# Kernel tuning notes

Measured on AMD Instinct MI355X. Metric: run time of the kernel, lower is better.

The kernel has to match this reference:

```python
import jax, jax.numpy as jnp
import numpy as np

WD, WH, WW = 6, 6, 6
NUM_HEADS = 8
EPS = 1e-5


def setup_inputs() -> dict:
    key = jax.random.key(0)
    ks = jax.random.split(key, 4)
    B, C, D, H, W = 1, 128, 48, 48, 48
    return {
        "q_map": jax.random.normal(ks[0], (B, C, D, H, W), dtype=jnp.float32),
        "k_map": jax.random.normal(ks[1], (B, C, D, H, W), dtype=jnp.float32),
        "v_map": jax.random.normal(ks[2], (B, C, D, H, W), dtype=jnp.float32),
        "gamma_q": jnp.ones((C,), jnp.float32),
        "beta_q": jnp.zeros((C,), jnp.float32),
        "gamma_kv": jnp.ones((C,), jnp.float32),
        "beta_kv": jnp.zeros((C,), jnp.float32),
        "proj_w": jax.random.normal(ks[3], (C, C), dtype=jnp.float32) * (1.0 / np.sqrt(C)),
        "proj_b": jnp.zeros((C,), jnp.float32),
    }


def _layernorm(x, g, b):
    m = jnp.mean(x, axis=-1, keepdims=True)
    v = jnp.mean(jnp.square(x - m), axis=-1, keepdims=True)
    return (x - m) * jax.lax.rsqrt(v + EPS) * g + b


def _window_partition(x):
    # x: (B, D, H, W, C) -> windows: (B*nD*nH*nW, wd*wh*ww, C)
    B, D, H, W, C = x.shape
    pd, ph, pw = (WD - D % WD) % WD, (WH - H % WH) % WH, (WW - W % WW) % WW
    if pd or ph or pw:
        x = jnp.pad(x, ((0, 0), (0, pd), (0, ph), (0, pw), (0, 0)))
    Dp, Hp, Wp = D + pd, H + ph, W + pw
    x = x.reshape(B, Dp // WD, WD, Hp // WH, WH, Wp // WW, WW, C)
    x = jnp.transpose(x, (0, 1, 3, 5, 2, 4, 6, 7))
    return x.reshape(-1, WD * WH * WW, C), (D, H, W, Dp, Hp, Wp)


def _window_reverse(windows, meta):
    D, H, W, Dp, Hp, Wp = meta
    C = windows.shape[-1]
    nD, nH, nW = Dp // WD, Hp // WH, Wp // WW
    B = windows.shape[0] // (nD * nH * nW)
    x = windows.reshape(B, nD, nH, nW, WD, WH, WW, C)
    x = jnp.transpose(x, (0, 1, 4, 2, 5, 3, 6, 7)).reshape(B, Dp, Hp, Wp, C)
    return x[:, :D, :H, :W, :]


def reference(q_map, k_map, v_map, gamma_q, beta_q, gamma_kv, beta_kv, proj_w, proj_b):
    # (B, C, D, H, W) -> (B, D, H, W, C)
    q_map = jnp.transpose(q_map, (0, 2, 3, 4, 1))
    k_map = jnp.transpose(k_map, (0, 2, 3, 4, 1))
    v_map = jnp.transpose(v_map, (0, 2, 3, 4, 1))

    q, meta = _window_partition(q_map)
    k, _ = _window_partition(k_map)
    v, _ = _window_partition(v_map)

    q = _layernorm(q, gamma_q, beta_q)
    k = _layernorm(k, gamma_kv, beta_kv)
    v = _layernorm(v, gamma_kv, beta_kv)

    Bw, Nq, C = q.shape
    dh = C // NUM_HEADS
    q = q.reshape(Bw, Nq, NUM_HEADS, dh)
    k = k.reshape(Bw, -1, NUM_HEADS, dh)
    v = v.reshape(Bw, -1, NUM_HEADS, dh)

    scale = 1.0 / np.sqrt(dh).astype(np.float32)
    scores = jnp.einsum("bqhd,bkhd->bhqk", q, k) * scale  # (Bw, h, Nq, Nk)
    attn = jax.nn.softmax(scores, axis=-1)
    out = jnp.einsum("bhqk,bkhd->bqhd", attn, v).reshape(Bw, Nq, C)

    out = out @ proj_w.T + proj_b
    out = _window_reverse(out, meta)
    return jnp.transpose(out, (0, 4, 1, 2, 3))  # (B, C, D, H, W)
```

## Files before the change

### kernel.cpp

```cpp
#include <hip/hip_runtime.h>
#include <hip/hip_bf16.h>

typedef short s16x8 __attribute__((ext_vector_type(8)));
typedef float f32x2 __attribute__((ext_vector_type(2)));
typedef float f32x4 __attribute__((ext_vector_type(4)));
typedef float f32x16 __attribute__((ext_vector_type(16)));
typedef unsigned int u32;
typedef unsigned short u16;
typedef u32 u32x4v __attribute__((ext_vector_type(4)));

#define TOK 216
#define THREADS 448
#define SP 110592
#define BUF0 0
#define VOFF 57344
#define WOFF 122880
#define GBOFF 155648
#define LDS_BYTES 157696

__device__ __forceinline__ u32 pack2(float a, float b) {
  u16 lo = __builtin_bit_cast(u16, __float2bfloat16(a));
  u16 hi = __builtin_bit_cast(u16, __float2bfloat16(b));
  return (u32)lo | ((u32)hi << 16);
}
__device__ __forceinline__ int swz(int row, int inner) {
  return inner ^ ((row & 7) << 4);
}

__device__ __forceinline__ void ln_stats(const f32x2* xv, float& mA, float& rA,
                                         float& mB, float& rB) {
  float sA = 0.f, s2A = 0.f, sB = 0.f, s2B = 0.f;
#pragma unroll
  for (int c = 0; c < 32; ++c) {
    sA += xv[c].x; s2A += xv[c].x * xv[c].x;
    sB += xv[c].y; s2B += xv[c].y * xv[c].y;
  }
  sA += __shfl_xor(sA, 1); s2A += __shfl_xor(s2A, 1);
  sB += __shfl_xor(sB, 1); s2B += __shfl_xor(s2B, 1);
  sA += __shfl_xor(sA, 2); s2A += __shfl_xor(s2A, 2);
  sB += __shfl_xor(sB, 2); s2B += __shfl_xor(s2B, 2);
  mA = sA * (1.0f / 128.0f);
  rA = rsqrtf(s2A * (1.0f / 128.0f) - mA * mA + 1e-5f);
  mB = sB * (1.0f / 128.0f);
  rB = rsqrtf(s2B * (1.0f / 128.0f) - mB * mB + 1e-5f);
}

template<bool MASK>
__device__ __forceinline__ void attn_step(const char* smem, int h, int kt,
                                          s16x8 qfh, int lane,
                                          f32x16& acc, float& lsum) {
  const int half = lane >> 5;
  const int krow = kt * 32 + (lane & 31);
  s16x8 kf = *(const s16x8*)(smem + BUF0 + krow * 256 +
                             swz(krow, h * 32 + half * 16));
  __builtin_amdgcn_s_setprio(1);
  f32x16 st = __builtin_amdgcn_mfma_f32_32x32x16_bf16(kf, qfh, (f32x16){}, 0, 0, 0);
  __builtin_amdgcn_s_setprio(0);
  const int vrow = h * 16 + (lane & 15);
  s16x8 vf0 = *(const s16x8*)(smem + VOFF + vrow * 512 +
                              swz(vrow, kt * 64 + half * 16));
  s16x8 vf1 = *(const s16x8*)(smem + VOFF + vrow * 512 +
                              swz(vrow, kt * 64 + 32 + half * 16));
  const int NR = MASK ? 12 : 16;
  u32 A[8];
  float ts = 0.f;
#pragma unroll
  for (int i = 0; i < 8; ++i) {
    float p0 = (2 * i < NR) ? __expf(st[2 * i]) : 0.f;
    float p1 = (2 * i + 1 < NR) ? __expf(st[2 * i + 1]) : 0.f;
    ts += p0 + p1;
    A[i] = pack2(p0, p1);
  }
  lsum += ts;
  s16x8 pf0 = __builtin_bit_cast(s16x8, (u32x4v){A[0], A[1], A[2], A[3]});
  s16x8 pf1 = __builtin_bit_cast(s16x8, (u32x4v){A[4], A[5], A[6], A[7]});
  __builtin_amdgcn_s_setprio(1);
  acc = __builtin_amdgcn_mfma_f32_32x32x16_bf16(vf0, pf0, acc, 0, 0, 0);
  acc = __builtin_amdgcn_mfma_f32_32x32x16_bf16(vf1, pf1, acc, 0, 0, 0);
  __builtin_amdgcn_s_setprio(0);
}

extern "C" __global__ __launch_bounds__(THREADS, 2)
void ca3d_kernel(const float* __restrict__ qm, const float* __restrict__ km,
                 const float* __restrict__ vm,
                 const float* __restrict__ gq, const float* __restrict__ bq,
                 const float* __restrict__ gkv, const float* __restrict__ bkv,
                 const float* __restrict__ pw, const float* __restrict__ pb,
                 float* __restrict__ out) {
  extern __shared__ __align__(16) char smem[];
  const int tid = threadIdx.x;
  const int lane = tid & 63;
  const int wv = tid >> 6;
  const int bid = blockIdx.x;
  const int wid = ((bid & 7) << 6) | (bid >> 3);
  const int wd = wid >> 6, wh = (wid >> 3) & 7, ww = wid & 7;
  const int boff = wd * 6 * 2304 + wh * 6 * 48 + ww * 6;

  for (int i = tid * 16; i < VOFF + 65536; i += THREADS * 16)
    *(f32x4*)(smem + i) = (f32x4){};
  if (tid < 128) {
    ((float*)(smem + GBOFF))[tid] = gq[tid];
    ((float*)(smem + GBOFF + 512))[tid] = bq[tid];
    ((float*)(smem + GBOFF + 1024))[tid] = gkv[tid];
    ((float*)(smem + GBOFF + 1536))[tid] = bkv[tid];
  }

  const bool lnAct = tid < 432;
  const int tp = tid >> 2;
  const int cbase = (tid & 3) * 32;
  const int tA = tp * 2, tB = tA + 1;
  int td = tA / 36, tr_ = tA - td * 36;
  int th_ = tr_ / 6, tw_ = tr_ - th_ * 6;
  const int gpos = boff + td * 2304 + th_ * 48 + tw_;
  const int vposA = (tA & ~0xC) | ((tA & 4) << 1) | ((tA & 8) >> 1);

  f32x2 qv[32], kv[32], vv[32];
  if (lnAct) {
#pragma unroll
    for (int c = 0; c < 32; ++c)
      qv[c] = *(const f32x2*)(qm + gpos + (cbase + c) * SP);
#pragma unroll
    for (int c = 0; c < 32; ++c)
      kv[c] = *(const f32x2*)(km + gpos + (cbase + c) * SP);
  }
  __syncthreads();

  const float* gql = (const float*)(smem + GBOFF);
  const float* bql = (const float*)(smem + GBOFF + 512);
  const float* gkl = (const float*)(smem + GBOFF + 1024);
  const float* bkl = (const float*)(smem + GBOFF + 1536);

  if (lnAct) {
    float mA, rA, mB, rB;
    ln_stats(qv, mA, rA, mB, rB);
#pragma unroll
    for (int c = 0; c < 32; c += 2) {
      int cc = cbase + c;
      float g0 = gql[cc], g1 = gql[cc + 1], b0 = bql[cc], b1 = bql[cc + 1];
      *(u32*)(smem + BUF0 + tA * 256 + swz(tA, cc * 2)) =
          pack2(((qv[c].x - mA) * rA * g0 + b0) * 0.25f,
                ((qv[c + 1].x - mA) * rA * g1 + b1) * 0.25f);
      *(u32*)(smem + BUF0 + tB * 256 + swz(tB, cc * 2)) =
          pack2(((qv[c].y - mB) * rB * g0 + b0) * 0.25f,
                ((qv[c + 1].y - mB) * rB * g1 + b1) * 0.25f);
    }
#pragma unroll
    for (int c = 0; c < 32; ++c)
      vv[c] = *(const f32x2*)(vm + gpos + (cbase + c) * SP);
  }
  __syncthreads();

  s16x8 qf[8];
  {
    int row = wv * 32 + (lane & 31);
    int ib = (lane >> 5) * 16;
#pragma unroll
    for (int h = 0; h < 8; ++h)
      qf[h] = *(const s16x8*)(smem + BUF0 + row * 256 + swz(row, h * 32 + ib));
  }
  __syncthreads();

  if (lnAct) {
    {
      float mA, rA, mB, rB;
      ln_stats(kv, mA, rA, mB, rB);
#pragma unroll
      for (int c = 0; c < 32; c += 2) {
        int cc = cbase + c;
        float g0 = gkl[cc], g1 = gkl[cc + 1], b0 = bkl[cc], b1 = bkl[cc + 1];
        *(u32*)(smem + BUF0 + tA * 256 + swz(tA, cc * 2)) =
            pack2((kv[c].x - mA) * rA * g0 + b0,
                  (kv[c + 1].x - mA) * rA * g1 + b1);
        *(u32*)(smem + BUF0 + tB * 256 + swz(tB, cc * 2)) =
            pack2((kv[c].y - mB) * rB * g0 + b0,
                  (kv[c + 1].y - mB) * rB * g1 + b1);
      }
    }
    {
      float mA, rA, mB, rB;
      ln_stats(vv, mA, rA, mB, rB);
#pragma unroll
      for (int c = 0; c < 32; ++c) {
        int cc = cbase + c;
        float g0 = gkl[cc], b0 = bkl[cc];
        *(u32*)(smem + VOFF + cc * 512 + swz(cc, vposA * 2)) =
            pack2((vv[c].x - mA) * rA * g0 + b0,
                  (vv[c].y - mB) * rB * g0 + b0);
      }
    }
  }
  for (int i = tid; i < 8192; i += THREADS) {
    int j = i >> 6, c2 = i & 63;
    f32x2 w2 = *(const f32x2*)(pw + j * 128 + c2 * 2);
    *(u32*)(smem + WOFF + j * 256 + swz(j, c2 * 4)) = pack2(w2.x, w2.y);
  }
  __syncthreads();

  u32 oPk[8][4];
#pragma unroll
  for (int hp = 0; hp < 4; ++hp) {
    const int h0 = hp * 2, h1 = h0 + 1;
    f32x16 a0 = {}, a1 = {};
    float l0 = 0.f, l1 = 0.f;
#pragma unroll 1
    for (int kt = 0; kt < 6; ++kt) {
      attn_step<false>(smem, h0, kt, qf[h0], lane, a0, l0);
      attn_step<false>(smem, h1, kt, qf[h1], lane, a1, l1);
    }
    attn_step<true>(smem, h0, 6, qf[h0], lane, a0, l0);
    attn_step<true>(smem, h1, 6, qf[h1], lane, a1, l1);
    l0 += __shfl_xor(l0, 32);
    l1 += __shfl_xor(l1, 32);
    float i0 = 1.0f / l0, i1 = 1.0f / l1;
#pragma unroll
    for (int r = 0; r < 4; ++r) {
      oPk[h0][r] = pack2(a0[2 * r] * i0, a0[2 * r + 1] * i0);
      oPk[h1][r] = pack2(a1[2 * r] * i1, a1[2 * r + 1] * i1);
    }
  }
  __syncthreads();

  {
    const int tok = wv * 32 + (lane & 31);
    const int half = lane >> 5;
#pragma unroll
    for (int h = 0; h < 8; ++h) {
      int chb = h * 32 + half * 8;
      *(u32*)(smem + BUF0 + tok * 256 + swz(tok, chb))      = oPk[h][0];
      *(u32*)(smem + BUF0 + tok * 256 + swz(tok, chb + 4))  = oPk[h][1];
      *(u32*)(smem + BUF0 + tok * 256 + swz(tok, chb + 16)) = oPk[h][2];
      *(u32*)(smem + BUF0 + tok * 256 + swz(tok, chb + 20)) = oPk[h][3];
    }
  }
  __syncthreads();

#pragma unroll 1
  for (int ti = 0; ti < 2; ++ti) {
    int tt = wv * 2 + ti;
    int tok = tt * 16 + (lane & 15);
    s16x8 bfr[4];
#pragma unroll
    for (int kk = 0; kk < 4; ++kk)
      bfr[kk] = *(const s16x8*)(smem + BUF0 + tok * 256 +
                                swz(tok, kk * 64 + (lane >> 4) * 16));
    bool tokValid = tok < TOK;
    int tdd = tok / 36, trr = tok - tdd * 36;
    int thh = trr / 6, tww = trr - thh * 6;
    int pos = boff + tdd * 2304 + thh * 48 + tww;
#pragma unroll 1
    for (int jt = 0; jt < 8; ++jt) {
      f32x4 acc = {};
#pragma unroll
      for (int kk = 0; kk < 4; ++kk) {
        int rw = jt * 16 + (lane & 15);
        s16x8 af = *(const s16x8*)(smem + WOFF + rw * 256 +
                                   swz(rw, kk * 64 + (lane >> 4) * 16));
        acc = __builtin_amdgcn_mfma_f32_16x16x32_bf16(af, bfr[kk], acc, 0, 0, 0);
      }
      f32x4 pbv = *(const f32x4*)(pb + jt * 16 + (lane >> 4) * 4);
      if (tokValid) {
#pragma unroll
        for (int r = 0; r < 4; ++r) {
          int j = jt * 16 + (lane >> 4) * 4 + r;
          out[j * SP + pos] = acc[r] + pbv[r];
        }
      }
    }
  }
}

extern "C" void kernel_launch(void* const* d_in, const int* in_sizes, int n_in,
                              void* d_out, int out_size, void* d_ws, size_t ws_size,
                              hipStream_t stream) {
  const float* qm  = (const float*)d_in[0];
  const float* km  = (const float*)d_in[1];
  const float* vm  = (const float*)d_in[2];
  const float* gq  = (const float*)d_in[3];
  const float* bq  = (const float*)d_in[4];
  const float* gkv = (const float*)d_in[5];
  const float* bkv = (const float*)d_in[6];
  const float* pw  = (const float*)d_in[7];
  const float* pb  = (const float*)d_in[8];
  hipLaunchKernelGGL(ca3d_kernel, dim3(512), dim3(THREADS), LDS_BYTES, stream,
                     qm, km, vm, gq, bq, gkv, bkv, pw, pb, (float*)d_out);
}
```

Measured before the change: 142.3 us.

## Split LayerNorm into bf16 pre-pass kernel and attention kernel with direct-to-LDS loads

Adds a pre-pass kernel that reads the fp32 channel-major q/k/v maps coalesced through shared memory, applies LayerNorm, and writes token-major bf16 tensors plus a bf16 projection weight into the workspace. The attention kernel then fills LDS with 16-byte global_load_lds copies, transposing V in LDS and zeroing its padding, instead of doing strided fp32 loads and LayerNorm in registers. The goal is better coalescing and fewer registers in the attention kernel. In exchange, roughly 85 MB of bf16 intermediates are written and read back, and a second kernel launch is added. The original fused kernel is kept as a fallback when the workspace is too small.

```diff
diff --git a/kernel.cpp b/kernel.cpp
--- a/kernel.cpp
+++ b/kernel.cpp
@@ -16,7 +16,10 @@
 #define VOFF 57344
 #define WOFF 122880
 #define GBOFF 155648
-#define LDS_BYTES 157696
+#define LDS_OLD 157696
+#define LDS_NEW 155648
+#define TENB 28311552ull
+#define WSNEED (3ull*TENB + 32768ull)
 
 __device__ __forceinline__ u32 pack2(float a, float b) {
   u16 lo = __builtin_bit_cast(u16, __float2bfloat16(a));
@@ -25,6 +28,11 @@
 }
 __device__ __forceinline__ int swz(int row, int inner) {
   return inner ^ ((row & 7) << 4);
+}
+__device__ __forceinline__ void gload16(const void* g, void* l) {
+  __builtin_amdgcn_global_load_lds(
+      (const __attribute__((address_space(1))) void*)g,
+      (__attribute__((address_space(3))) void*)l, 16, 0, 0);
 }
 
 __device__ __forceinline__ void ln_stats(const f32x2* xv, float& mA, float& rA,
@@ -80,6 +88,234 @@
   __builtin_amdgcn_s_setprio(0);
 }
 
+extern "C" __global__ __launch_bounds__(256)
+void lnpre_kernel(const float* __restrict__ qm, const float* __restrict__ km,
+                  const float* __restrict__ vm,
+                  const float* __restrict__ gq, const float* __restrict__ bq,
+                  const float* __restrict__ gkv, const float* __restrict__ bkv,
+                  const float* __restrict__ pw,
+                  u16* __restrict__ qn, u16* __restrict__ kn,
+                  u16* __restrict__ vn, u16* __restrict__ wbf) {
+  const int tid = threadIdx.x;
+  const int bid = blockIdx.x;
+  if (bid >= 2304) {
+#pragma unroll
+    for (int k = 0; k < 32; ++k) {
+      int idx = tid + 256 * k;
+      f32x2 w2 = *(const f32x2*)(pw + idx * 2);
+      ((u32*)wbf)[idx] = pack2(w2.x, w2.y);
+    }
+    return;
+  }
+  __shared__ float lf[6144];
+  __shared__ float gb[512];
+  const int d = bid / 48, h = bid - d * 48;
+  const int dh = d * 2304 + h * 48;
+  if (tid < 128) {
+    gb[tid] = gq[tid]; gb[128 + tid] = bq[tid];
+    gb[256 + tid] = gkv[tid]; gb[384 + tid] = bkv[tid];
+  }
+  const int w = tid >> 2, q = tid & 3;
+#pragma unroll 1
+  for (int t = 0; t < 3; ++t) {
+    const float* src = t == 0 ? qm : (t == 1 ? km : vm);
+    u16* dst = t == 0 ? qn : (t == 1 ? kn : vn);
+    const float* g = (t == 0) ? gb : gb + 256;
+    const float* b = (t == 0) ? gb + 128 : gb + 384;
+    const float scale = (t == 0) ? 0.25f : 1.0f;
+#pragma unroll
+    for (int k = 0; k < 6; ++k) {
+      int j = tid + 256 * k;
+      int ch = j / 12, wq = j - ch * 12;
+      *(f32x4*)(lf + ch * 48 + wq * 4) =
+          *(const f32x4*)(src + (long)ch * SP + dh + wq * 4);
+    }
+    __syncthreads();
+    if (tid < 192) {
+      float s = 0.f, s2 = 0.f;
+#pragma unroll
+      for (int c = 0; c < 32; ++c) {
+        float x = lf[(q + 4 * c) * 48 + w];
+        s += x; s2 += x * x;
+      }
+      s += __shfl_xor(s, 1); s2 += __shfl_xor(s2, 1);
+      s += __shfl_xor(s, 2); s2 += __shfl_xor(s2, 2);
+      float m = s * (1.f / 128.f);
+      float r = rsqrtf(s2 * (1.f / 128.f) - m * m + 1e-5f);
+      u32* op = (u32*)(dst + (long)(dh + w) * 128 + 32 * q);
+#pragma unroll
+      for (int cc = 0; cc < 32; cc += 2) {
+        int ch = 32 * q + cc;
+        float y0 = ((lf[ch * 48 + w] - m) * r * g[ch] + b[ch]) * scale;
+        float y1 = ((lf[(ch + 1) * 48 + w] - m) * r * g[ch + 1] + b[ch + 1]) * scale;
+        op[cc >> 1] = pack2(y0, y1);
+      }
+    }
+    __syncthreads();
+  }
+}
+
+extern "C" __global__ __launch_bounds__(THREADS, 2)
+void attn2_kernel(const u16* __restrict__ qn, const u16* __restrict__ kn,
+                  const u16* __restrict__ vn, const u16* __restrict__ wbf,
+                  const float* __restrict__ pb, float* __restrict__ out) {
+  extern __shared__ __align__(16) char smem[];
+  const int tid = threadIdx.x;
+  const int lane = tid & 63;
+  const int wv = tid >> 6;
+  const int bid = blockIdx.x;
+  const int wid = ((bid & 7) << 6) | (bid >> 3);
+  const int wd = wid >> 6, wh = (wid >> 3) & 7, ww = wid & 7;
+  const int wd6 = wd * 6, wh6 = wh * 6, ww6 = ww * 6;
+  const int boff = wd6 * 2304 + wh6 * 48 + ww6;
+
+  for (int uu = wv; uu < 140; uu += 7) {
+    const u16* s; char* d;
+    if (uu < 54) {
+      int u = uu, row = 4 * u + (lane >> 4);
+      int tq = row / 6;
+      int g = (wd6 + tq / 6) * 2304 + (wh6 + tq % 6) * 48 + ww6 + row % 6;
+      s = qn + g * 128 + (((lane & 15) ^ (row & 7)) << 3);
+      d = smem + BUF0 + u * 1024;
+    } else if (uu < 108) {
+      int u = uu - 54, row = 4 * u + (lane >> 4);
+      int tq = row / 6;
+      int g = (wd6 + tq / 6) * 2304 + (wh6 + tq % 6) * 48 + ww6 + row % 6;
+      s = vn + g * 128 + ((lane & 15) << 3);
+      d = smem + VOFF + u * 1024;
+    } else {
+      int u = uu - 108, row = 4 * u + (lane >> 4);
+      s = wbf + row * 128 + (((lane & 15) ^ (row & 7)) << 3);
+      d = smem + WOFF + u * 1024;
+    }
+    gload16(s, d);
+  }
+  __syncthreads();
+
+  s16x8 qf[8];
+  {
+    int row = wv * 32 + (lane & 31);
+    int ib = (lane >> 5) * 16;
+#pragma unroll
+    for (int h = 0; h < 8; ++h)
+      qf[h] = *(const s16x8*)(smem + BUF0 + row * 256 + swz(row, h * 32 + ib));
+  }
+  __syncthreads();
+
+  for (int uu = wv; uu < 54; uu += 7) {
+    int row = 4 * uu + (lane >> 4);
+    int tq = row / 6;
+    int g = (wd6 + tq / 6) * 2304 + (wh6 + tq % 6) * 48 + ww6 + row % 6;
+    gload16(kn + g * 128 + (((lane & 15) ^ (row & 7)) << 3),
+            smem + BUF0 + uu * 1024);
+  }
+  u32 tr[32];
+#pragma unroll
+  for (int k = 0; k < 16; ++k) {
+    int u = tid + 448 * k;
+    if (u < 6912) {
+      int t = (u >> 6) * 2, c2 = u & 63;
+      tr[2 * k]     = *(const u32*)(smem + VOFF + t * 256 + c2 * 4);
+      tr[2 * k + 1] = *(const u32*)(smem + VOFF + t * 256 + 256 + c2 * 4);
+    }
+  }
+  __syncthreads();
+
+#pragma unroll
+  for (int k = 0; k < 16; ++k) {
+    int u = tid + 448 * k;
+    if (u < 6912) {
+      int t = (u >> 6) * 2, c2 = u & 63;
+      int st = (t & ~12) | ((t & 4) << 1) | ((t & 8) >> 1);
+      int c = 2 * c2;
+      u32 w0 = (tr[2 * k] & 0xFFFFu) | (tr[2 * k + 1] << 16);
+      u32 w1 = (tr[2 * k] >> 16) | (tr[2 * k + 1] & 0xFFFF0000u);
+      *(u32*)(smem + VOFF + c * 512 + ((st * 2) ^ ((c & 7) << 4))) = w0;
+      *(u32*)(smem + VOFF + (c + 1) * 512 + ((st * 2) ^ (((c + 1) & 7) << 4))) = w1;
+    }
+  }
+  if (tid < 128) {
+    int x = (tid & 7) << 4;
+    *(u32*)(smem + VOFF + tid * 512 + (424 ^ x)) = 0;
+    *(u32*)(smem + VOFF + tid * 512 + (428 ^ x)) = 0;
+    *(u32*)(smem + VOFF + tid * 512 + (440 ^ x)) = 0;
+    *(u32*)(smem + VOFF + tid * 512 + (444 ^ x)) = 0;
+  }
+  __syncthreads();
+
+  u32 oPk[8][4];
+#pragma unroll
+  for (int hp = 0; hp < 4; ++hp) {
+    const int h0 = hp * 2, h1 = h0 + 1;
+    f32x16 a0 = {}, a1 = {};
+    float l0 = 0.f, l1 = 0.f;
+#pragma unroll 1
+    for (int kt = 0; kt < 6; ++kt) {
+      attn_step<false>(smem, h0, kt, qf[h0], lane, a0, l0);
+      attn_step<false>(smem, h1, kt, qf[h1], lane, a1, l1);
+    }
+    attn_step<true>(smem, h0, 6, qf[h0], lane, a0, l0);
+    attn_step<true>(smem, h1, 6, qf[h1], lane, a1, l1);
+    l0 += __shfl_xor(l0, 32);
+    l1 += __shfl_xor(l1, 32);
+    float i0 = 1.0f / l0, i1 = 1.0f / l1;
+#pragma unroll
+    for (int r = 0; r < 4; ++r) {
+      oPk[h0][r] = pack2(a0[2 * r] * i0, a0[2 * r + 1] * i0);
+      oPk[h1][r] = pack2(a1[2 * r] * i1, a1[2 * r + 1] * i1);
+    }
+  }
+  __syncthreads();
+
+  {
+    const int tok = wv * 32 + (lane & 31);
+    const int half = lane >> 5;
+#pragma unroll
+    for (int h = 0; h < 8; ++h) {
+      int chb = h * 32 + half * 8;
+      *(u32*)(smem + BUF0 + tok * 256 + swz(tok, chb))      = oPk[h][0];
+      *(u32*)(smem + BUF0 + tok * 256 + swz(tok, chb + 4))  = oPk[h][1];
+      *(u32*)(smem + BUF0 + tok * 256 + swz(tok, chb + 16)) = oPk[h][2];
+      *(u32*)(smem + BUF0 + tok * 256 + swz(tok, chb + 20)) = oPk[h][3];
+    }
+  }
+  __syncthreads();
+
+#pragma unroll 1
+  for (int ti = 0; ti < 2; ++ti) {
+    int tt = wv * 2 + ti;
+    int tok = tt * 16 + (lane & 15);
+    s16x8 bfr[4];
+#pragma unroll
+    for (int kk = 0; kk < 4; ++kk)
+      bfr[kk] = *(const s16x8*)(smem + BUF0 + tok * 256 +
+                                swz(tok, kk * 64 + (lane >> 4) * 16));
+    bool tokValid = tok < TOK;
+    int tdd = tok / 36, trr = tok - tdd * 36;
+    int thh = trr / 6, tww = trr - thh * 6;
+    int pos = boff + tdd * 2304 + thh * 48 + tww;
+#pragma unroll 1
+    for (int jt = 0; jt < 8; ++jt) {
+      f32x4 acc = {};
+#pragma unroll
+      for (int kk = 0; kk < 4; ++kk) {
+        int rw = jt * 16 + (lane & 15);
+        s16x8 af = *(const s16x8*)(smem + WOFF + rw * 256 +
+                                   swz(rw, kk * 64 + (lane >> 4) * 16));
+        acc = __builtin_amdgcn_mfma_f32_16x16x32_bf16(af, bfr[kk], acc, 0, 0, 0);
+      }
+      f32x4 pbv = *(const f32x4*)(pb + jt * 16 + (lane >> 4) * 4);
+      if (tokValid) {
+#pragma unroll
+        for (int r = 0; r < 4; ++r) {
+          int j = jt * 16 + (lane >> 4) * 4 + r;
+          out[j * SP + pos] = acc[r] + pbv[r];
+        }
+      }
+    }
+  }
+}
+
 extern "C" __global__ __launch_bounds__(THREADS, 2)
 void ca3d_kernel(const float* __restrict__ qm, const float* __restrict__ km,
                  const float* __restrict__ vm,
@@ -104,7 +340,6 @@
     ((float*)(smem + GBOFF + 1024))[tid] = gkv[tid];
     ((float*)(smem + GBOFF + 1536))[tid] = bkv[tid];
   }
-
   const bool lnAct = tid < 432;
   const int tp = tid >> 2;
   const int cbase = (tid & 3) * 32;
@@ -124,12 +359,10 @@
       kv[c] = *(const f32x2*)(km + gpos + (cbase + c) * SP);
   }
   __syncthreads();
-
   const float* gql = (const float*)(smem + GBOFF);
   const float* bql = (const float*)(smem + GBOFF + 512);
   const float* gkl = (const float*)(smem + GBOFF + 1024);
   const float* bkl = (const float*)(smem + GBOFF + 1536);
-
   if (lnAct) {
     float mA, rA, mB, rB;
     ln_stats(qv, mA, rA, mB, rB);
@@ -149,7 +382,6 @@
       vv[c] = *(const f32x2*)(vm + gpos + (cbase + c) * SP);
   }
   __syncthreads();
-
   s16x8 qf[8];
   {
     int row = wv * 32 + (lane & 31);
@@ -159,7 +391,6 @@
       qf[h] = *(const s16x8*)(smem + BUF0 + row * 256 + swz(row, h * 32 + ib));
   }
   __syncthreads();
-
   if (lnAct) {
     {
       float mA, rA, mB, rB;
@@ -195,7 +426,6 @@
     *(u32*)(smem + WOFF + j * 256 + swz(j, c2 * 4)) = pack2(w2.x, w2.y);
   }
   __syncthreads();
-
   u32 oPk[8][4];
 #pragma unroll
   for (int hp = 0; hp < 4; ++hp) {
@@ -219,7 +449,6 @@
     }
   }
   __syncthreads();
-
   {
     const int tok = wv * 32 + (lane & 31);
     const int half = lane >> 5;
@@ -233,7 +462,6 @@
     }
   }
   __syncthreads();
-
 #pragma unroll 1
   for (int ti = 0; ti < 2; ++ti) {
     int tt = wv * 2 + ti;
@@ -281,6 +509,17 @@
   const float* bkv = (const float*)d_in[6];
   const float* pw  = (const float*)d_in[7];
   const float* pb  = (const float*)d_in[8];
-  hipLaunchKernelGGL(ca3d_kernel, dim3(512), dim3(THREADS), LDS_BYTES, stream,
-                     qm, km, vm, gq, bq, gkv, bkv, pw, pb, (float*)d_out);
-}
+  if (ws_size >= WSNEED) {
+    u16* qn  = (u16*)d_ws;
+    u16* kn  = (u16*)((char*)d_ws + TENB);
+    u16* vn  = (u16*)((char*)d_ws + 2 * TENB);
+    u16* wbf = (u16*)((char*)d_ws + 3 * TENB);
+    hipLaunchKernelGGL(lnpre_kernel, dim3(2305), dim3(256), 0, stream,
+                       qm, km, vm, gq, bq, gkv, bkv, pw, qn, kn, vn, wbf);
+    hipLaunchKernelGGL(attn2_kernel, dim3(512), dim3(THREADS), LDS_NEW, stream,
+                       qn, kn, vn, wbf, pb, (float*)d_out);
+  } else {
+    hipLaunchKernelGGL(ca3d_kernel, dim3(512), dim3(THREADS), LDS_OLD, stream,
+                       qm, km, vm, gq, bq, gkv, bkv, pw, pb, (float*)d_out);
+  }
+}
```

Result: slower. 155.7 us (+9.4%).
